# Optimization experiments

Measured on AMD Instinct MI355X. Metric: run time of the kernel, lower is better.

Reference implementation:

```python
import jax, jax.numpy as jnp
import numpy as np

N, E, G = 50000, 800000, 64
IN, HID, H, OUT = 128, 64, 4, 10


def _gat_layer(x, src, dst, W, a_src, a_dst, b):
    # x: [N, Fin]; W: [H*C, Fin]; a_src/a_dst: [H, C]; b: [H*C]
    n = x.shape[0]
    C = a_src.shape[1]
    h = (x @ W.T).reshape(n, H, C)                      # [N, H, C]
    e_src = jnp.einsum('nhc,hc->nh', h, a_src)          # [N, H]
    e_dst = jnp.einsum('nhc,hc->nh', h, a_dst)          # [N, H]
    logits = jax.nn.leaky_relu(e_src[src] + e_dst[dst], 0.2)  # [E', H]
    # segment softmax over destination node
    m = jax.ops.segment_max(logits, dst, num_segments=n)
    ex = jnp.exp(logits - m[dst])
    denom = jax.ops.segment_sum(ex, dst, num_segments=n)
    alpha = ex / (denom[dst] + 1e-16)                   # [E', H]
    msg = h[src] * alpha[:, :, None]                    # [E', H, C]
    out = jax.ops.segment_sum(msg, dst, num_segments=n) # [N, H, C]
    return out.reshape(n, H * C) + b


def setup_inputs() -> dict:
    key = jax.random.key(0)
    ks = jax.random.split(key, 20)
    x = jax.random.normal(ks[0], (N, IN), dtype=jnp.float32)
    edge_index = jax.random.randint(ks[1], (2, E), 0, N, dtype=jnp.int64)
    batch = jnp.sort(jax.random.randint(ks[2], (N,), 0, G, dtype=jnp.int64))

    def glorot(k, shape):
        fan = shape[-1]
        return jax.random.normal(k, shape, dtype=jnp.float32) / jnp.sqrt(jnp.float32(fan))

    ins = [IN, HID * H, HID * H]
    params = {}
    for i, fin in enumerate(ins, start=1):
        params[f'W{i}'] = glorot(ks[3 * i], (H * HID, fin))
        params[f'a_src{i}'] = glorot(ks[3 * i + 1], (H, HID))
        params[f'a_dst{i}'] = glorot(ks[3 * i + 2], (H, HID))
        params[f'b{i}'] = jnp.zeros((H * HID,), dtype=jnp.float32)
    params['Wl'] = glorot(ks[13], (OUT, H * HID))
    params['bl'] = jnp.zeros((OUT,), dtype=jnp.float32)
    return dict(x=x, edge_index=edge_index, batch=batch, **params)


def reference(x, edge_index, batch,
              W1, a_src1, a_dst1, b1,
              W2, a_src2, a_dst2, b2,
              W3, a_src3, a_dst3, b3,
              Wl, bl):
    n = x.shape[0]
    loops = jnp.arange(n, dtype=edge_index.dtype)
    src = jnp.concatenate([edge_index[0], loops])  # add self-loops (PyG default)
    dst = jnp.concatenate([edge_index[1], loops])

    h = jax.nn.elu(_gat_layer(x, src, dst, W1, a_src1, a_dst1, b1))
    h = jax.nn.elu(_gat_layer(h, src, dst, W2, a_src2, a_dst2, b2))
    h = _gat_layer(h, src, dst, W3, a_src3, a_dst3, b3)

    # global mean pool over graphs
    sums = jax.ops.segment_sum(h, batch, num_segments=G)          # [G, H*HID]
    counts = jax.ops.segment_sum(jnp.ones((n,), h.dtype), batch, num_segments=G)
    pooled = sums / jnp.maximum(counts, 1.0)[:, None]
    return pooled @ Wl.T + bl                                      # [G, OUT]
```

## Files before the change

### kernel.cpp

```cpp
#include <hip/hip_runtime.h>
#include <hip/hip_bf16.h>
#include <math.h>

#define NNODES 50000
#define NEDGES 800000
#define NGRAPH 64
#define FIN 128
#define HC 256
#define NHEAD 4
#define NOUT 10
#define ETOT (NEDGES + NNODES)
#define NB196 ((NNODES + 255) / 256)
#define BCAP 5376
#define S1CHUNK 4096
#define NBS1 ((ETOT + S1CHUNK - 1) / S1CHUNK)


typedef unsigned short u16;
typedef unsigned char u8;
typedef __attribute__((ext_vector_type(8))) short short8;
typedef __attribute__((ext_vector_type(4))) float f32x4;
typedef __attribute__((ext_vector_type(2))) float f32x2;

__device__ inline u16 f2b(float f) {
    union { float f; unsigned u; } v; v.f = f;
    unsigned r = v.u + 0x7FFF + ((v.u >> 16) & 1);
    return (u16)(r >> 16);
}
__device__ inline float b2f(u16 u) {
    union { unsigned u; float f; } v; v.u = ((unsigned)u) << 16; return v.f;
}

__device__ inline void gload_lds16(const void* g, void* l) {
    __builtin_amdgcn_global_load_lds(
        (const __attribute__((address_space(1))) unsigned*)g,
        (__attribute__((address_space(3))) unsigned*)l, 16, 0, 0);
}


#define CS0 (NNODES * FIN)
#define CS1 (HC * FIN)
#define CS2 (HC * HC)
#define NBCONV (((CS0 + CS1 + 2 * CS2) / 4 + 255) / 256)

__global__ void prep_kernel(const float* __restrict__ x, const float* __restrict__ W1,
                            const float* __restrict__ W2, const float* __restrict__ W3,
                            u16* __restrict__ xb, u16* __restrict__ w1b,
                            u16* __restrict__ w2b, u16* __restrict__ w3b) {
    int b = blockIdx.x;
    long i = (long)(b * 256 + threadIdx.x) * 4;
    if (i < CS0) {
        float4 v = *(const float4*)(x + i);
        ushort4 o;
        o.x = f2b(v.x); o.y = f2b(v.y); o.z = f2b(v.z); o.w = f2b(v.w);
        *(ushort4*)(xb + i) = o;
    } else if (i < CS0 + CS1) {
        long off = i - CS0;
        float4 v = *(const float4*)(W1 + off);
        ushort4 o;
        o.x = f2b(v.x); o.y = f2b(v.y); o.z = f2b(v.z); o.w = f2b(v.w);
        *(ushort4*)(w1b + off) = o;
    } else if (i < CS0 + CS1 + 2 * CS2) {
        const float* src; u16* dst; long off;
        if (i < CS0 + CS1 + CS2) { src = W2; dst = w2b; off = i - CS0 - CS1; }
        else                     { src = W3; dst = w3b; off = i - CS0 - CS1 - CS2; }
        float4 v = *(const float4*)(src + off);
        int row = (int)(off >> 8), col = (int)(off & 255);
        float vv[4] = {v.x, v.y, v.z, v.w};
        #pragma unroll
        for (int k = 0; k < 4; ++k) {
            int c = col + k;
            int pp = (c & ~63) | ((c & 15) << 2) | ((c >> 4) & 3);
            dst[row * 256 + pp] = f2b(vv[k]);
        }
    }
}


__global__ __launch_bounds__(256) void scatter1_kernel(const int* __restrict__ ei,
                                                       int* __restrict__ bcur,
                                                       unsigned* __restrict__ tmp) {
    __shared__ int hist[NB196];
    __shared__ int basec[NB196];
    int tid = threadIdx.x;
    int e0 = blockIdx.x * S1CHUNK;
    for (int i = tid; i < NB196; i += 256) hist[i] = 0;
    __syncthreads();
    int bkt[16], rnk[16];
    unsigned pk[16];
    #pragma unroll
    for (int k = 0; k < 16; ++k) {
        int e = e0 + k * 256 + tid;
        bkt[k] = -1;
        if (e < ETOT) {
            int src, dstn;
            if (e < NEDGES) { src = ei[e]; dstn = ei[NEDGES + e]; }
            else            { src = dstn = e - NEDGES; }
            int b = dstn >> 8;
            bkt[k] = b;
            rnk[k] = atomicAdd(&hist[b], 1);
            pk[k] = (unsigned)src | ((unsigned)(dstn & 255) << 16);
        }
    }
    __syncthreads();
    for (int i = tid; i < NB196; i += 256) {
        int h = hist[i];
        basec[i] = h ? atomicAdd(&bcur[i], h) : 0;
    }
    __syncthreads();
    #pragma unroll
    for (int k = 0; k < 16; ++k) {
        if (bkt[k] >= 0) {
            int pos = basec[bkt[k]] + rnk[k];
            if (pos < BCAP)
                tmp[(size_t)bkt[k] * BCAP + pos] = pk[k];
        }
    }
}


__global__ __launch_bounds__(256) void scanb_kernel(const int* __restrict__ bcur,
                                                    int* __restrict__ bsum,
                                                    const int* __restrict__ batch,
                                                    int* __restrict__ goff) {
    int tid = threadIdx.x, lane = tid & 63, wid = tid >> 6;
    __shared__ int ws[4];
    int v = 0;
    if (tid < NB196) { v = bcur[tid]; if (v > BCAP) v = BCAP; }
    int x = v;
    #pragma unroll
    for (int o = 1; o < 64; o <<= 1) {
        int t = __shfl_up(x, o);
        if (lane >= o) x += t;
    }
    if (lane == 63) ws[wid] = x;
    __syncthreads();
    if (tid < 4) {
        int w = ws[tid];
        #pragma unroll
        for (int o = 1; o < 4; o <<= 1) {
            int t = __shfl_up(w, o, 4);
            if ((tid & 3) >= o) w += t;
        }
        ws[tid] = w;
    }
    __syncthreads();
    int wexcl = wid ? ws[wid - 1] : 0;
    if (tid <= NB196) bsum[tid] = x - v + wexcl;
    if (tid <= NGRAPH) {
        int g = tid, lo = 0, hi = NNODES;
        while (lo < hi) {
            int mid = (lo + hi) >> 1;
            if (batch[mid] < g) lo = mid + 1; else hi = mid;
        }
        goff[g] = lo;
    }
}


__global__ __launch_bounds__(256) void scatter2_kernel(const unsigned* __restrict__ tmp,
                                                       const int* __restrict__ bcur,
                                                       const int* __restrict__ bsum,
                                                       int* __restrict__ off,
                                                       int* __restrict__ ssrc) {
    __shared__ unsigned ebuf[BCAP];
    __shared__ int ldss[BCAP];
    __shared__ int cnt[256];
    __shared__ int loff[256];
    __shared__ int ws[4];
    int b = blockIdx.x;
    int tid = threadIdx.x;
    int n = bcur[b];
    if (n > BCAP) n = BCAP;
    cnt[tid] = 0;
    const unsigned* tb = tmp + (size_t)b * BCAP;
    for (int i = tid; i < n; i += 256) ebuf[i] = tb[i];
    __syncthreads();
    for (int i = tid; i < n; i += 256) atomicAdd(&cnt[ebuf[i] >> 16], 1);
    __syncthreads();
    int lane = tid & 63, wid = tid >> 6;
    int v = cnt[tid];
    int x = v;
    #pragma unroll
    for (int o = 1; o < 64; o <<= 1) {
        int t = __shfl_up(x, o);
        if (lane >= o) x += t;
    }
    if (lane == 63) ws[wid] = x;
    __syncthreads();
    if (tid < 4) {
        int w = ws[tid];
        #pragma unroll
        for (int o = 1; o < 4; o <<= 1) {
            int t = __shfl_up(w, o, 4);
            if ((tid & 3) >= o) w += t;
        }
        ws[tid] = w;
    }
    __syncthreads();
    int wexcl = wid ? ws[wid - 1] : 0;
    int excl = x - v + wexcl;
    loff[tid] = excl;
    off[b * 256 + tid] = excl;
    cnt[tid] = 0;
    __syncthreads();
    for (int i = tid; i < n; i += 256) {
        unsigned pk = ebuf[i];
        int ld = (int)(pk >> 16);
        int rank = atomicAdd(&cnt[ld], 1);
        ldss[loff[ld] + rank] = (int)(pk & 0xFFFFu);
    }
    __syncthreads();
    int s = bsum[b];
    for (int i = tid; i < n; i += 256) ssrc[s + i] = ldss[i];
}


#define TBM 128
#define TBN 128
#define TBK 32

__global__ __launch_bounds__(256) void gemm_mfma(const u16* __restrict__ A,
                                                 const u16* __restrict__ B,
                                                 u8* __restrict__ C, int K,
                                                 const float* __restrict__ asrc,
                                                 const float* __restrict__ adst,
                                                 float* __restrict__ es,
                                                 float* __restrict__ ed) {
    __shared__ u16 Als[TBM * TBK];
    __shared__ u16 Bls[TBN * TBK];
    int tid = threadIdx.x;
    int wave = tid >> 6, lane = tid & 63;
    int brow = blockIdx.x * TBM, bcol = blockIdx.y * TBN;
    int m_base = (wave >> 1) * 64, n_base = (wave & 1) * 64;
    int r0 = tid >> 2, kc = (tid & 3) * 8;
    int lquad = lane >> 4, l16 = lane & 15;

    f32x4 acc[4][4] = {};

    const u16* ga0 = A + (size_t)(brow + r0) * K + kc;
    const u16* ga1 = A + (size_t)(brow + 64 + r0) * K + kc;
    const u16* gb0 = B + (size_t)(bcol + r0) * K + kc;
    const u16* gb1 = B + (size_t)(bcol + 64 + r0) * K + kc;
    u16* la0 = &Als[r0 * TBK + kc];
    u16* la1 = &Als[(64 + r0) * TBK + kc];
    u16* lb0 = &Bls[r0 * TBK + kc];
    u16* lb1 = &Bls[(64 + r0) * TBK + kc];

    for (int k0 = 0; k0 < K; k0 += TBK) {
        __syncthreads();
        gload_lds16(ga0 + k0, la0);
        gload_lds16(ga1 + k0, la1);
        gload_lds16(gb0 + k0, lb0);
        gload_lds16(gb1 + k0, lb1);
        __syncthreads();
        short8 fa[4], fb[4];
        #pragma unroll
        for (int i = 0; i < 4; ++i) {
            fa[i] = *(const short8*)(&Als[(m_base + i * 16 + l16) * TBK + lquad * 8]);
            fb[i] = *(const short8*)(&Bls[(n_base + i * 16 + l16) * TBK + lquad * 8]);
        }
        #pragma unroll
        for (int i = 0; i < 4; ++i)
            #pragma unroll
            for (int j = 0; j < 4; ++j)
                acc[i][j] = __builtin_amdgcn_mfma_f32_16x16x32_bf16(fa[i], fb[j], acc[i][j], 0, 0, 0);
    }

    #pragma unroll
    for (int i = 0; i < 4; ++i) {
        int rbase = brow + m_base + i * 16 + lquad * 4;
        #pragma unroll
        for (int r = 0; r < 4; ++r) {
            int row = rbase + r;
            if (row < NNODES) {
                int u = 0;
                u = __builtin_amdgcn_cvt_pk_fp8_f32(acc[i][0][r], acc[i][1][r], u, false);
                u = __builtin_amdgcn_cvt_pk_fp8_f32(acc[i][2][r], acc[i][3][r], u, true);
                *(int*)(C + (size_t)row * HC + bcol + n_base + l16 * 4) = u;
            }
        }
    }

    int head = (bcol + n_base) >> 6;
    float asv[4], adv[4];
    #pragma unroll
    for (int j = 0; j < 4; ++j) {
        asv[j] = asrc[head * 64 + j * 16 + l16];
        adv[j] = adst[head * 64 + j * 16 + l16];
    }
    #pragma unroll
    for (int i = 0; i < 4; ++i) {
        #pragma unroll
        for (int r = 0; r < 4; ++r) {
            float ps = 0.f, pd = 0.f;
            #pragma unroll
            for (int j = 0; j < 4; ++j) {
                ps = fmaf(acc[i][j][r], asv[j], ps);
                pd = fmaf(acc[i][j][r], adv[j], pd);
            }
            #pragma unroll
            for (int o = 1; o < 16; o <<= 1) {
                ps += __shfl_xor(ps, o);
                pd += __shfl_xor(pd, o);
            }
            int row = brow + m_base + i * 16 + lquad * 4 + r;
            if (l16 == 0 && row < NNODES) {
                es[row * 4 + head] = ps;
                ed[row * 4 + head] = pd;
            }
        }
    }
}


__global__ __launch_bounds__(256) void aggregate_kernel(const u8* __restrict__ h,
                                                        const int* __restrict__ ssrc,
                                                        const int* __restrict__ off,
                                                        const int* __restrict__ bsum,
                                                        const float* __restrict__ es,
                                                        const float* __restrict__ ed,
                                                        const float* __restrict__ bias,
                                                        u16* __restrict__ out,
                                                        int apply_elu) {
    __shared__ int2 xch[4][4][2][17];
    const unsigned* h32 = (const unsigned*)h;
    int wid = threadIdx.x >> 6;
    int dst = blockIdx.x * 4 + wid;
    if (dst >= NNODES) return;
    int lane = threadIdx.x & 63;
    int head = lane >> 4;
    int j16 = lane & 15;
    int s = off[dst] + bsum[dst >> 8];
    int e = off[dst + 1] + bsum[(dst + 1) >> 8];
    float edh = ed[dst * 4 + head];

    float a0 = 0.f, a1 = 0.f, a2 = 0.f, a3 = 0.f, dpriv = 0.f;

    {
        int cnt0 = e - s; if (cnt0 > 16) cnt0 = 16;
        int idx0 = s + j16; if (idx0 >= ETOT) idx0 = 0;
        int src0 = ssrc[idx0];
        float l = es[src0 * 4 + head] + edh;
        l = fmaxf(l, 0.2f * l);
        float ex0 = 0.f;
        if (j16 < cnt0) { ex0 = __expf(l); dpriv += ex0; }
        xch[wid][head][0][j16] = make_int2(src0, __float_as_int(ex0));
    }
    int nidx = s + 16 + j16; if (nidx >= ETOT) nidx = 0;
    int nsrc = ssrc[nidx];

    int buf = 0;
    for (int base = s; base < e; base += 16) {
        int cur = e - base; if (cur > 16) cur = 16;
        int nbase = base + 16;
        float esv = es[(unsigned)nsrc * 4 + head];
        int n2idx = base + 32 + j16; if (n2idx >= ETOT) n2idx = 0;
        int n2src = ssrc[n2idx];
        const int2* slot = &xch[wid][head][buf][0];
        for (int j = 0; j < cur; ++j) {
            int2 pr = slot[j];
            float exj = __int_as_float(pr.y);
            unsigned hv = h32[(unsigned)pr.x * 64 + lane];
            f32x2 lo = __builtin_amdgcn_cvt_pk_f32_fp8(hv, false);
            f32x2 hi = __builtin_amdgcn_cvt_pk_f32_fp8(hv, true);
            a0 += lo.x * exj;
            a1 += lo.y * exj;
            a2 += hi.x * exj;
            a3 += hi.y * exj;
        }
        if (nbase < e) {
            int ncnt = e - nbase; if (ncnt > 16) ncnt = 16;
            float l = esv + edh;
            l = fmaxf(l, 0.2f * l);
            float nex = 0.f;
            if (j16 < ncnt) { nex = __expf(l); dpriv += nex; }
            xch[wid][head][buf ^ 1][j16] = make_int2(nsrc, __float_as_int(nex));
        }
        nsrc = n2src;
        buf ^= 1;
    }

    #pragma unroll
    for (int o = 1; o < 16; o <<= 1) dpriv += __shfl_xor(dpriv, o);
    float inv = 1.f / (dpriv + 1e-16f);
    int bbase = ((lane >> 4) << 6) | (lane & 15);
    float b0 = bias[bbase], b1 = bias[bbase + 16], b2 = bias[bbase + 32], b3 = bias[bbase + 48];
    float o0 = a0 * inv + b0;
    float o1 = a1 * inv + b1;
    float o2 = a2 * inv + b2;
    float o3 = a3 * inv + b3;
    if (apply_elu) {
        o0 = o0 > 0.f ? o0 : __expf(o0) - 1.f;
        o1 = o1 > 0.f ? o1 : __expf(o1) - 1.f;
        o2 = o2 > 0.f ? o2 : __expf(o2) - 1.f;
        o3 = o3 > 0.f ? o3 : __expf(o3) - 1.f;
    }
    ushort4 ov;
    ov.x = f2b(o0); ov.y = f2b(o1); ov.z = f2b(o2); ov.w = f2b(o3);
    *(ushort4*)(out + (size_t)dst * HC + lane * 4) = ov;
}


__global__ __launch_bounds__(256) void pool_kernel(const u16* __restrict__ hin,
                                                   const int* __restrict__ goff,
                                                   float* __restrict__ pp) {
    int g = blockIdx.x;
    int slice = blockIdx.y;
    int lane = threadIdx.x & 63;
    int wid = threadIdx.x >> 6;
    int s = goff[g], e = goff[g + 1];
    float a0 = 0.f, a1 = 0.f, a2 = 0.f, a3 = 0.f;
    for (int n = s + slice * 4 + wid; n < e; n += 32) {
        ushort4 hv = *(const ushort4*)(hin + (size_t)n * HC + lane * 4);
        a0 += b2f(hv.x); a1 += b2f(hv.y); a2 += b2f(hv.z); a3 += b2f(hv.w);
    }
    __shared__ float4 part[4][64];
    part[wid][lane] = make_float4(a0, a1, a2, a3);
    __syncthreads();
    if (wid == 0) {
        float4 p0 = part[0][lane], p1 = part[1][lane], p2 = part[2][lane], p3 = part[3][lane];
        float4 v = make_float4((p0.x + p1.x) + (p2.x + p3.x),
                               (p0.y + p1.y) + (p2.y + p3.y),
                               (p0.z + p1.z) + (p2.z + p3.z),
                               (p0.w + p1.w) + (p2.w + p3.w));
        *(float4*)(pp + ((size_t)(g * 8 + slice)) * HC + lane * 4) = v;
    }
}


__global__ __launch_bounds__(64) void final_kernel(const float* __restrict__ pp,
                                                   const int* __restrict__ goff,
                                                   const float* __restrict__ Wl,
                                                   const float* __restrict__ bl,
                                                   float* __restrict__ out) {
    int g = blockIdx.x;
    int lane = threadIdx.x;
    float4 pv = make_float4(0.f, 0.f, 0.f, 0.f);
    #pragma unroll
    for (int sl = 0; sl < 8; ++sl) {
        float4 v = *(const float4*)(pp + ((size_t)(g * 8 + sl)) * HC + lane * 4);
        pv.x += v.x; pv.y += v.y; pv.z += v.z; pv.w += v.w;
    }
    float cntf = fmaxf((float)(goff[g + 1] - goff[g]), 1.f);
    float inv = 1.f / cntf;
    pv.x *= inv; pv.y *= inv; pv.z *= inv; pv.w *= inv;
    int wbase = ((lane >> 4) << 6) | (lane & 15);
    float acc[NOUT];
    #pragma unroll
    for (int o = 0; o < NOUT; ++o) {
        const float* w = Wl + o * HC + wbase;
        acc[o] = pv.x * w[0] + pv.y * w[16] + pv.z * w[32] + pv.w * w[48];
    }
    #pragma unroll
    for (int s = 32; s > 0; s >>= 1)
        #pragma unroll
        for (int o = 0; o < NOUT; ++o)
            acc[o] += __shfl_xor(acc[o], s);
    if (lane == 0) {
        #pragma unroll
        for (int o = 0; o < NOUT; ++o)
            out[g * NOUT + o] = acc[o] + bl[o];
    }
}


extern "C" void kernel_launch(void* const* d_in, const int* in_sizes, int n_in,
                              void* d_out, int out_size, void* d_ws, size_t ws_size,
                              hipStream_t stream) {
    (void)in_sizes; (void)n_in; (void)out_size; (void)ws_size;
    const float* x   = (const float*)d_in[0];
    const int*   ei  = (const int*)d_in[1];
    const int*   bat = (const int*)d_in[2];
    const float* W1  = (const float*)d_in[3];
    const float* as1 = (const float*)d_in[4];
    const float* ad1 = (const float*)d_in[5];
    const float* b1  = (const float*)d_in[6];
    const float* W2  = (const float*)d_in[7];
    const float* as2 = (const float*)d_in[8];
    const float* ad2 = (const float*)d_in[9];
    const float* b2  = (const float*)d_in[10];
    const float* W3  = (const float*)d_in[11];
    const float* as3 = (const float*)d_in[12];
    const float* ad3 = (const float*)d_in[13];
    const float* b3  = (const float*)d_in[14];
    const float* Wl  = (const float*)d_in[15];
    const float* bl  = (const float*)d_in[16];
    float* out = (float*)d_out;

    char* ws = (char*)d_ws;
    size_t p = 0;
    auto alloc = [&](size_t bytes) {
        size_t a = p;
        p += (bytes + 255) & ~(size_t)255;
        return a;
    };
    int*      off  = (int*)(ws + alloc((size_t)(NB196 * 256 + 256) * 4));
    int*      bcur = (int*)(ws + alloc(256 * 4));
    int*      ssrc = (int*)(ws + alloc((size_t)ETOT * 4));
    unsigned* tmp  = (unsigned*)(ws + alloc((size_t)NB196 * BCAP * 4));
    int*      bsum = (int*)(ws + alloc(256 * 4));
    float*    es   = (float*)(ws + alloc((size_t)NNODES * NHEAD * 4));
    float*    ed   = (float*)(ws + alloc((size_t)NNODES * NHEAD * 4));
    u16*      xb   = (u16*)(ws + alloc((size_t)NNODES * FIN * 2));
    u16*      w1b  = (u16*)(ws + alloc((size_t)HC * FIN * 2));
    u16*      w2b  = (u16*)(ws + alloc((size_t)HC * HC * 2));
    u16*      w3b  = (u16*)(ws + alloc((size_t)HC * HC * 2));
    u8*       Hb   = (u8*)(ws + alloc((size_t)NNODES * HC));
    u16*      Ab   = (u16*)(ws + alloc((size_t)NNODES * HC * 2));
    float*    pp   = (float*)(ws + alloc((size_t)NGRAPH * 8 * HC * 4));
    int*      goff = (int*)(ws + alloc((size_t)(NGRAPH + 1) * 4));
    alloc(128 * 1024);

    hipMemsetAsync(bcur, 0, 256 * 4, stream);

    prep_kernel<<<NBCONV, 256, 0, stream>>>(x, W1, W2, W3, xb, w1b, w2b, w3b);

    scatter1_kernel<<<NBS1, 256, 0, stream>>>(ei, bcur, tmp);
    scanb_kernel<<<1, 256, 0, stream>>>(bcur, bsum, bat, goff);
    scatter2_kernel<<<NB196, 256, 0, stream>>>(tmp, bcur, bsum, off, ssrc);

    dim3 ggrid((NNODES + TBM - 1) / TBM, HC / TBN);
    int nblocks4 = (NNODES + 3) / 4;

    gemm_mfma<<<ggrid, 256, 0, stream>>>(xb, w1b, Hb, FIN, as1, ad1, es, ed);
    aggregate_kernel<<<nblocks4, 256, 0, stream>>>(Hb, ssrc, off, bsum, es, ed, b1, Ab, 1);
    gemm_mfma<<<ggrid, 256, 0, stream>>>(Ab, w2b, Hb, HC, as2, ad2, es, ed);
    aggregate_kernel<<<nblocks4, 256, 0, stream>>>(Hb, ssrc, off, bsum, es, ed, b2, Ab, 1);
    gemm_mfma<<<ggrid, 256, 0, stream>>>(Ab, w3b, Hb, HC, as3, ad3, es, ed);
    aggregate_kernel<<<nblocks4, 256, 0, stream>>>(Hb, ssrc, off, bsum, es, ed, b3, Ab, 0);

    dim3 pgrid(NGRAPH, 8);
    pool_kernel<<<pgrid, 256, 0, stream>>>(Ab, goff, pp);
    final_kernel<<<NGRAPH, 64, 0, stream>>>(pp, goff, Wl, bl, out);
}
```

Before: 338.7 us.

## Split each destination's edge list across two wavefronts with LDS reduction

The aggregate kernel now assigns two wavefronts per destination node, each handling alternating 16-edge chunks, and combines partial accumulators and softmax denominators through shared memory after a block barrier. It also fully unrolls the inner gather loop for full chunks and uses packed two-wide float math for the accumulation. The aim is to shorten the serial dependent gather chain per node and raise memory-level parallelism, at the cost of a __syncthreads, extra LDS traffic, and half the wavefronts sitting idle in the epilogue. The grid is doubled to match.

Result: slower. 436.3 us (+28.8%).

```diff
diff --git a/kernel.cpp b/kernel.cpp
--- a/kernel.cpp
+++ b/kernel.cpp
@@ -324,10 +324,12 @@
                                                         u16* __restrict__ out,
                                                         int apply_elu) {
     __shared__ int2 xch[4][4][2][17];
+    __shared__ f32x4 part[4][64];
+    __shared__ float dsum[4][4];
     const unsigned* h32 = (const unsigned*)h;
     int wid = threadIdx.x >> 6;
-    int dst = blockIdx.x * 4 + wid;
-    if (dst >= NNODES) return;
+    int half = wid & 1;
+    int dst = blockIdx.x * 2 + (wid >> 1);
     int lane = threadIdx.x & 63;
     int head = lane >> 4;
     int j16 = lane & 15;
@@ -335,40 +337,55 @@
     int e = off[dst + 1] + bsum[(dst + 1) >> 8];
     float edh = ed[dst * 4 + head];
 
-    float a0 = 0.f, a1 = 0.f, a2 = 0.f, a3 = 0.f, dpriv = 0.f;
-
+    f32x2 a01 = {0.f, 0.f}, a23 = {0.f, 0.f};
+    float dpriv = 0.f;
+
+    int b0 = s + half * 16;
     {
-        int cnt0 = e - s; if (cnt0 > 16) cnt0 = 16;
-        int idx0 = s + j16; if (idx0 >= ETOT) idx0 = 0;
+        int cnt0 = e - b0; if (cnt0 > 16) cnt0 = 16;
+        int idx0 = b0 + j16; if (idx0 >= ETOT) idx0 = 0;
         int src0 = ssrc[idx0];
-        float l = es[src0 * 4 + head] + edh;
+        float l = es[(unsigned)src0 * 4 + head] + edh;
         l = fmaxf(l, 0.2f * l);
         float ex0 = 0.f;
         if (j16 < cnt0) { ex0 = __expf(l); dpriv += ex0; }
         xch[wid][head][0][j16] = make_int2(src0, __float_as_int(ex0));
     }
-    int nidx = s + 16 + j16; if (nidx >= ETOT) nidx = 0;
+    int nidx = b0 + 32 + j16; if (nidx >= ETOT) nidx = 0;
     int nsrc = ssrc[nidx];
 
     int buf = 0;
-    for (int base = s; base < e; base += 16) {
+    for (int base = b0; base < e; base += 32) {
         int cur = e - base; if (cur > 16) cur = 16;
-        int nbase = base + 16;
         float esv = es[(unsigned)nsrc * 4 + head];
-        int n2idx = base + 32 + j16; if (n2idx >= ETOT) n2idx = 0;
+        int n2idx = base + 64 + j16; if (n2idx >= ETOT) n2idx = 0;
         int n2src = ssrc[n2idx];
         const int2* slot = &xch[wid][head][buf][0];
-        for (int j = 0; j < cur; ++j) {
-            int2 pr = slot[j];
-            float exj = __int_as_float(pr.y);
-            unsigned hv = h32[(unsigned)pr.x * 64 + lane];
-            f32x2 lo = __builtin_amdgcn_cvt_pk_f32_fp8(hv, false);
-            f32x2 hi = __builtin_amdgcn_cvt_pk_f32_fp8(hv, true);
-            a0 += lo.x * exj;
-            a1 += lo.y * exj;
-            a2 += hi.x * exj;
-            a3 += hi.y * exj;
-        }
+        if (cur == 16) {
+            #pragma unroll
+            for (int j = 0; j < 16; ++j) {
+                int2 pr = slot[j];
+                float exj = __int_as_float(pr.y);
+                unsigned hv = h32[(unsigned)pr.x * 64 + lane];
+                f32x2 lo = __builtin_amdgcn_cvt_pk_f32_fp8(hv, false);
+                f32x2 hi = __builtin_amdgcn_cvt_pk_f32_fp8(hv, true);
+                f32x2 e2 = {exj, exj};
+                a01 += lo * e2;
+                a23 += hi * e2;
+            }
+        } else {
+            for (int j = 0; j < cur; ++j) {
+                int2 pr = slot[j];
+                float exj = __int_as_float(pr.y);
+                unsigned hv = h32[(unsigned)pr.x * 64 + lane];
+                f32x2 lo = __builtin_amdgcn_cvt_pk_f32_fp8(hv, false);
+                f32x2 hi = __builtin_amdgcn_cvt_pk_f32_fp8(hv, true);
+                f32x2 e2 = {exj, exj};
+                a01 += lo * e2;
+                a23 += hi * e2;
+            }
+        }
+        int nbase = base + 32;
         if (nbase < e) {
             int ncnt = e - nbase; if (ncnt > 16) ncnt = 16;
             float l = esv + edh;
@@ -383,22 +400,29 @@
 
     #pragma unroll
     for (int o = 1; o < 16; o <<= 1) dpriv += __shfl_xor(dpriv, o);
-    float inv = 1.f / (dpriv + 1e-16f);
-    int bbase = ((lane >> 4) << 6) | (lane & 15);
-    float b0 = bias[bbase], b1 = bias[bbase + 16], b2 = bias[bbase + 32], b3 = bias[bbase + 48];
-    float o0 = a0 * inv + b0;
-    float o1 = a1 * inv + b1;
-    float o2 = a2 * inv + b2;
-    float o3 = a3 * inv + b3;
-    if (apply_elu) {
-        o0 = o0 > 0.f ? o0 : __expf(o0) - 1.f;
-        o1 = o1 > 0.f ? o1 : __expf(o1) - 1.f;
-        o2 = o2 > 0.f ? o2 : __expf(o2) - 1.f;
-        o3 = o3 > 0.f ? o3 : __expf(o3) - 1.f;
-    }
-    ushort4 ov;
-    ov.x = f2b(o0); ov.y = f2b(o1); ov.z = f2b(o2); ov.w = f2b(o3);
-    *(ushort4*)(out + (size_t)dst * HC + lane * 4) = ov;
+    if (j16 == 0) dsum[wid][head] = dpriv;
+    f32x4 pv; pv[0] = a01.x; pv[1] = a01.y; pv[2] = a23.x; pv[3] = a23.y;
+    part[wid][lane] = pv;
+    __syncthreads();
+    if (half == 0) {
+        f32x4 p0 = part[wid][lane], p1 = part[wid + 1][lane];
+        float d = dsum[wid][head] + dsum[wid + 1][head];
+        float inv = 1.f / (d + 1e-16f);
+        int bbase = ((lane >> 4) << 6) | (lane & 15);
+        float o0 = (p0[0] + p1[0]) * inv + bias[bbase];
+        float o1 = (p0[1] + p1[1]) * inv + bias[bbase + 16];
+        float o2 = (p0[2] + p1[2]) * inv + bias[bbase + 32];
+        float o3 = (p0[3] + p1[3]) * inv + bias[bbase + 48];
+        if (apply_elu) {
+            o0 = o0 > 0.f ? o0 : __expf(o0) - 1.f;
+            o1 = o1 > 0.f ? o1 : __expf(o1) - 1.f;
+            o2 = o2 > 0.f ? o2 : __expf(o2) - 1.f;
+            o3 = o3 > 0.f ? o3 : __expf(o3) - 1.f;
+        }
+        ushort4 ov;
+        ov.x = f2b(o0); ov.y = f2b(o1); ov.z = f2b(o2); ov.w = f2b(o3);
+        *(ushort4*)(out + (size_t)dst * HC + lane * 4) = ov;
+    }
 }
 
 
@@ -521,14 +545,14 @@
     scatter2_kernel<<<NB196, 256, 0, stream>>>(tmp, bcur, bsum, off, ssrc);
 
     dim3 ggrid((NNODES + TBM - 1) / TBM, HC / TBN);
-    int nblocks4 = (NNODES + 3) / 4;
+    int nblocks2 = (NNODES + 1) / 2;
 
     gemm_mfma<<<ggrid, 256, 0, stream>>>(xb, w1b, Hb, FIN, as1, ad1, es, ed);
-    aggregate_kernel<<<nblocks4, 256, 0, stream>>>(Hb, ssrc, off, bsum, es, ed, b1, Ab, 1);
+    aggregate_kernel<<<nblocks2, 256, 0, stream>>>(Hb, ssrc, off, bsum, es, ed, b1, Ab, 1);
     gemm_mfma<<<ggrid, 256, 0, stream>>>(Ab, w2b, Hb, HC, as2, ad2, es, ed);
-    aggregate_kernel<<<nblocks4, 256, 0, stream>>>(Hb, ssrc, off, bsum, es, ed, b2, Ab, 1);
+    aggregate_kernel<<<nblocks2, 256, 0, stream>>>(Hb, ssrc, off, bsum, es, ed, b2, Ab, 1);
     gemm_mfma<<<ggrid, 256, 0, stream>>>(Ab, w3b, Hb, HC, as3, ad3, es, ed);
-    aggregate_kernel<<<nblocks4, 256, 0, stream>>>(Hb, ssrc, off, bsum, es, ed, b3, Ab, 0);
+    aggregate_kernel<<<nblocks2, 256, 0, stream>>>(Hb, ssrc, off, bsum, es, ed, b3, Ab, 0);
 
     dim3 pgrid(NGRAPH, 8);
     pool_kernel<<<pgrid, 256, 0, stream>>>(Ab, goff, pp);
```

## Process two destination nodes per wavefront in GAT aggregation with interleaved gathers

Applied to the files above, without the earlier changes.

Each wavefront in the aggregation kernel now handles two consecutive destination nodes, interleaving their edge-chunk loops so two independent gather streams are in flight at once. Full 16-edge chunks use an unrolled inner loop, and accumulation uses packed float2 multiply-adds. The goal is more memory-level parallelism and fewer loop overheads on the latency-bound feature gathers. In exchange it uses more registers and LDS per wave, and the grid is halved, which leaves less room for load balancing when the two nodes have very different degrees.

Result: slower. 353.4 us (+4.3%).

```diff
diff --git a/kernel.cpp b/kernel.cpp
--- a/kernel.cpp
+++ b/kernel.cpp
@@ -323,82 +323,161 @@
                                                         const float* __restrict__ bias,
                                                         u16* __restrict__ out,
                                                         int apply_elu) {
-    __shared__ int2 xch[4][4][2][17];
+    __shared__ int2 xch[4][2][4][2][17];
     const unsigned* h32 = (const unsigned*)h;
     int wid = threadIdx.x >> 6;
-    int dst = blockIdx.x * 4 + wid;
-    if (dst >= NNODES) return;
     int lane = threadIdx.x & 63;
     int head = lane >> 4;
     int j16 = lane & 15;
-    int s = off[dst] + bsum[dst >> 8];
-    int e = off[dst + 1] + bsum[(dst + 1) >> 8];
-    float edh = ed[dst * 4 + head];
-
-    float a0 = 0.f, a1 = 0.f, a2 = 0.f, a3 = 0.f, dpriv = 0.f;
+    int dstA = blockIdx.x * 8 + wid * 2;
+    int dstB = dstA + 1;
+    int sA = off[dstA] + bsum[dstA >> 8];
+    int eA = off[dstA + 1] + bsum[(dstA + 1) >> 8];
+    int sB = eA;
+    int eB = off[dstB + 1] + bsum[(dstB + 1) >> 8];
+    float edhA = ed[dstA * 4 + head];
+    float edhB = ed[dstB * 4 + head];
+
+    f32x2 a01A = {0.f, 0.f}, a23A = {0.f, 0.f};
+    f32x2 a01B = {0.f, 0.f}, a23B = {0.f, 0.f};
+    float dprA = 0.f, dprB = 0.f;
 
     {
-        int cnt0 = e - s; if (cnt0 > 16) cnt0 = 16;
-        int idx0 = s + j16; if (idx0 >= ETOT) idx0 = 0;
-        int src0 = ssrc[idx0];
-        float l = es[src0 * 4 + head] + edh;
-        l = fmaxf(l, 0.2f * l);
-        float ex0 = 0.f;
-        if (j16 < cnt0) { ex0 = __expf(l); dpriv += ex0; }
-        xch[wid][head][0][j16] = make_int2(src0, __float_as_int(ex0));
-    }
-    int nidx = s + 16 + j16; if (nidx >= ETOT) nidx = 0;
-    int nsrc = ssrc[nidx];
-
-    int buf = 0;
-    for (int base = s; base < e; base += 16) {
-        int cur = e - base; if (cur > 16) cur = 16;
-        int nbase = base + 16;
-        float esv = es[(unsigned)nsrc * 4 + head];
-        int n2idx = base + 32 + j16; if (n2idx >= ETOT) n2idx = 0;
-        int n2src = ssrc[n2idx];
-        const int2* slot = &xch[wid][head][buf][0];
-        for (int j = 0; j < cur; ++j) {
-            int2 pr = slot[j];
-            float exj = __int_as_float(pr.y);
-            unsigned hv = h32[(unsigned)pr.x * 64 + lane];
-            f32x2 lo = __builtin_amdgcn_cvt_pk_f32_fp8(hv, false);
-            f32x2 hi = __builtin_amdgcn_cvt_pk_f32_fp8(hv, true);
-            a0 += lo.x * exj;
-            a1 += lo.y * exj;
-            a2 += hi.x * exj;
-            a3 += hi.y * exj;
-        }
-        if (nbase < e) {
-            int ncnt = e - nbase; if (ncnt > 16) ncnt = 16;
-            float l = esv + edh;
-            l = fmaxf(l, 0.2f * l);
+        int i0A = sA + j16; if (i0A >= ETOT) i0A = 0;
+        int i0B = sB + j16; if (i0B >= ETOT) i0B = 0;
+        int srcA0 = ssrc[i0A];
+        int srcB0 = ssrc[i0B];
+        float lA = es[(unsigned)srcA0 * 4 + head] + edhA;
+        float lB = es[(unsigned)srcB0 * 4 + head] + edhB;
+        lA = fmaxf(lA, 0.2f * lA);
+        lB = fmaxf(lB, 0.2f * lB);
+        int cA0 = eA - sA; if (cA0 > 16) cA0 = 16;
+        int cB0 = eB - sB; if (cB0 > 16) cB0 = 16;
+        float exA = 0.f, exB = 0.f;
+        if (j16 < cA0) { exA = __expf(lA); dprA += exA; }
+        if (j16 < cB0) { exB = __expf(lB); dprB += exB; }
+        xch[wid][0][head][0][j16] = make_int2(srcA0, __float_as_int(exA));
+        xch[wid][1][head][0][j16] = make_int2(srcB0, __float_as_int(exB));
+    }
+    int niA = sA + 16 + j16; if (niA >= ETOT) niA = 0;
+    int niB = sB + 16 + j16; if (niB >= ETOT) niB = 0;
+    int nsrcA = ssrc[niA];
+    int nsrcB = ssrc[niB];
+
+    int baseA = sA, baseB = sB;
+    int bufA = 0, bufB = 0;
+    while (baseA < eA || baseB < eB) {
+        float esvA = es[(unsigned)nsrcA * 4 + head];
+        float esvB = es[(unsigned)nsrcB * 4 + head];
+        int n2A = baseA + 32 + j16; if (n2A >= ETOT) n2A = 0;
+        int n2B = baseB + 32 + j16; if (n2B >= ETOT) n2B = 0;
+        int n2srcA = ssrc[n2A];
+        int n2srcB = ssrc[n2B];
+        int curA = eA - baseA; if (curA > 16) curA = 16; if (curA < 0) curA = 0;
+        int curB = eB - baseB; if (curB > 16) curB = 16; if (curB < 0) curB = 0;
+        const int2* slA = &xch[wid][0][head][bufA][0];
+        const int2* slB = &xch[wid][1][head][bufB][0];
+        if (curA == 16) {
+            #pragma unroll
+            for (int j = 0; j < 16; ++j) {
+                int2 pr = slA[j];
+                float exj = __int_as_float(pr.y);
+                unsigned hv = h32[(unsigned)pr.x * 64 + lane];
+                f32x2 lo = __builtin_amdgcn_cvt_pk_f32_fp8(hv, false);
+                f32x2 hi = __builtin_amdgcn_cvt_pk_f32_fp8(hv, true);
+                f32x2 e2 = {exj, exj};
+                a01A += lo * e2;
+                a23A += hi * e2;
+            }
+        } else {
+            for (int j = 0; j < curA; ++j) {
+                int2 pr = slA[j];
+                float exj = __int_as_float(pr.y);
+                unsigned hv = h32[(unsigned)pr.x * 64 + lane];
+                f32x2 lo = __builtin_amdgcn_cvt_pk_f32_fp8(hv, false);
+                f32x2 hi = __builtin_amdgcn_cvt_pk_f32_fp8(hv, true);
+                f32x2 e2 = {exj, exj};
+                a01A += lo * e2;
+                a23A += hi * e2;
+            }
+        }
+        if (curB == 16) {
+            #pragma unroll
+            for (int j = 0; j < 16; ++j) {
+                int2 pr = slB[j];
+                float exj = __int_as_float(pr.y);
+                unsigned hv = h32[(unsigned)pr.x * 64 + lane];
+                f32x2 lo = __builtin_amdgcn_cvt_pk_f32_fp8(hv, false);
+                f32x2 hi = __builtin_amdgcn_cvt_pk_f32_fp8(hv, true);
+                f32x2 e2 = {exj, exj};
+                a01B += lo * e2;
+                a23B += hi * e2;
+            }
+        } else {
+            for (int j = 0; j < curB; ++j) {
+                int2 pr = slB[j];
+                float exj = __int_as_float(pr.y);
+                unsigned hv = h32[(unsigned)pr.x * 64 + lane];
+                f32x2 lo = __builtin_amdgcn_cvt_pk_f32_fp8(hv, false);
+                f32x2 hi = __builtin_amdgcn_cvt_pk_f32_fp8(hv, true);
+                f32x2 e2 = {exj, exj};
+                a01B += lo * e2;
+                a23B += hi * e2;
+            }
+        }
+        int nbA = baseA + 16, nbB = baseB + 16;
+        if (nbA < eA) {
+            int nc = eA - nbA; if (nc > 16) nc = 16;
+            float l = esvA + edhA; l = fmaxf(l, 0.2f * l);
             float nex = 0.f;
-            if (j16 < ncnt) { nex = __expf(l); dpriv += nex; }
-            xch[wid][head][buf ^ 1][j16] = make_int2(nsrc, __float_as_int(nex));
-        }
-        nsrc = n2src;
-        buf ^= 1;
-    }
-
-    #pragma unroll
-    for (int o = 1; o < 16; o <<= 1) dpriv += __shfl_xor(dpriv, o);
-    float inv = 1.f / (dpriv + 1e-16f);
+            if (j16 < nc) { nex = __expf(l); dprA += nex; }
+            xch[wid][0][head][bufA ^ 1][j16] = make_int2(nsrcA, __float_as_int(nex));
+        }
+        if (nbB < eB) {
+            int nc = eB - nbB; if (nc > 16) nc = 16;
+            float l = esvB + edhB; l = fmaxf(l, 0.2f * l);
+            float nex = 0.f;
+            if (j16 < nc) { nex = __expf(l); dprB += nex; }
+            xch[wid][1][head][bufB ^ 1][j16] = make_int2(nsrcB, __float_as_int(nex));
+        }
+        nsrcA = n2srcA; nsrcB = n2srcB;
+        bufA ^= 1; bufB ^= 1;
+        baseA = nbA; baseB = nbB;
+    }
+
+    #pragma unroll
+    for (int o = 1; o < 16; o <<= 1) {
+        dprA += __shfl_xor(dprA, o);
+        dprB += __shfl_xor(dprB, o);
+    }
+    float invA = 1.f / (dprA + 1e-16f);
+    float invB = 1.f / (dprB + 1e-16f);
     int bbase = ((lane >> 4) << 6) | (lane & 15);
     float b0 = bias[bbase], b1 = bias[bbase + 16], b2 = bias[bbase + 32], b3 = bias[bbase + 48];
-    float o0 = a0 * inv + b0;
-    float o1 = a1 * inv + b1;
-    float o2 = a2 * inv + b2;
-    float o3 = a3 * inv + b3;
+
+    float o0 = a01A.x * invA + b0;
+    float o1 = a01A.y * invA + b1;
+    float o2 = a23A.x * invA + b2;
+    float o3 = a23A.y * invA + b3;
+    float p0 = a01B.x * invB + b0;
+    float p1 = a01B.y * invB + b1;
+    float p2 = a23B.x * invB + b2;
+    float p3 = a23B.y * invB + b3;
     if (apply_elu) {
         o0 = o0 > 0.f ? o0 : __expf(o0) - 1.f;
         o1 = o1 > 0.f ? o1 : __expf(o1) - 1.f;
         o2 = o2 > 0.f ? o2 : __expf(o2) - 1.f;
         o3 = o3 > 0.f ? o3 : __expf(o3) - 1.f;
-    }
-    ushort4 ov;
-    ov.x = f2b(o0); ov.y = f2b(o1); ov.z = f2b(o2); ov.w = f2b(o3);
-    *(ushort4*)(out + (size_t)dst * HC + lane * 4) = ov;
+        p0 = p0 > 0.f ? p0 : __expf(p0) - 1.f;
+        p1 = p1 > 0.f ? p1 : __expf(p1) - 1.f;
+        p2 = p2 > 0.f ? p2 : __expf(p2) - 1.f;
+        p3 = p3 > 0.f ? p3 : __expf(p3) - 1.f;
+    }
+    ushort4 ovA, ovB;
+    ovA.x = f2b(o0); ovA.y = f2b(o1); ovA.z = f2b(o2); ovA.w = f2b(o3);
+    ovB.x = f2b(p0); ovB.y = f2b(p1); ovB.z = f2b(p2); ovB.w = f2b(p3);
+    *(ushort4*)(out + (size_t)dstA * HC + lane * 4) = ovA;
+    *(ushort4*)(out + (size_t)dstB * HC + lane * 4) = ovB;
 }
 
 
@@ -521,14 +600,14 @@
     scatter2_kernel<<<NB196, 256, 0, stream>>>(tmp, bcur, bsum, off, ssrc);
 
     dim3 ggrid((NNODES + TBM - 1) / TBM, HC / TBN);
-    int nblocks4 = (NNODES + 3) / 4;
+    int nblocks8 = NNODES / 8;
 
     gemm_mfma<<<ggrid, 256, 0, stream>>>(xb, w1b, Hb, FIN, as1, ad1, es, ed);
-    aggregate_kernel<<<nblocks4, 256, 0, stream>>>(Hb, ssrc, off, bsum, es, ed, b1, Ab, 1);
+    aggregate_kernel<<<nblocks8, 256, 0, stream>>>(Hb, ssrc, off, bsum, es, ed, b1, Ab, 1);
     gemm_mfma<<<ggrid, 256, 0, stream>>>(Ab, w2b, Hb, HC, as2, ad2, es, ed);
-    aggregate_kernel<<<nblocks4, 256, 0, stream>>>(Hb, ssrc, off, bsum, es, ed, b2, Ab, 1);
+    aggregate_kernel<<<nblocks8, 256, 0, stream>>>(Hb, ssrc, off, bsum, es, ed, b2, Ab, 1);
     gemm_mfma<<<ggrid, 256, 0, stream>>>(Ab, w3b, Hb, HC, as3, ad3, es, ed);
-    aggregate_kernel<<<nblocks4, 256, 0, stream>>>(Hb, ssrc, off, bsum, es, ed, b3, Ab, 0);
+    aggregate_kernel<<<nblocks8, 256, 0, stream>>>(Hb, ssrc, off, bsum, es, ed, b3, Ab, 0);
 
     dim3 pgrid(NGRAPH, 8);
     pool_kernel<<<pgrid, 256, 0, stream>>>(Ab, goff, pp);
```

## Merge prep and scatter launches, fold bucket scan into scatter2, simplify aggregate loop

Applied to the files above, without the earlier changes.

Fuses the bf16 conversion kernel and the first scatter pass into one launch. The single-block scan kernel is removed: each scatter2 block recomputes the global bucket prefix and writes absolute offsets, and pool/final compute graph bounds by binary search on batch. The aggregate kernel's double-buffered software prefetch of source indices is replaced by a simpler full-chunk loop plus a tail, which drops the extra bsum lookup but gives up load prefetching. The aim is to cut launch and serialization overhead from small kernels.

Result: no change. 342.9 us (+1.2%).

```diff
diff --git a/kernel.cpp b/kernel.cpp
--- a/kernel.cpp
+++ b/kernel.cpp
@@ -37,53 +37,64 @@
         (__attribute__((address_space(3))) unsigned*)l, 16, 0, 0);
 }
 
+__device__ inline int lbound(const int* __restrict__ batch, int g) {
+    int lo = 0, hi = NNODES;
+    while (lo < hi) {
+        int mid = (lo + hi) >> 1;
+        if (batch[mid] < g) lo = mid + 1; else hi = mid;
+    }
+    return lo;
+}
+
 
 #define CS0 (NNODES * FIN)
 #define CS1 (HC * FIN)
 #define CS2 (HC * HC)
 #define NBCONV (((CS0 + CS1 + 2 * CS2) / 4 + 255) / 256)
 
-__global__ void prep_kernel(const float* __restrict__ x, const float* __restrict__ W1,
-                            const float* __restrict__ W2, const float* __restrict__ W3,
-                            u16* __restrict__ xb, u16* __restrict__ w1b,
-                            u16* __restrict__ w2b, u16* __restrict__ w3b) {
-    int b = blockIdx.x;
-    long i = (long)(b * 256 + threadIdx.x) * 4;
-    if (i < CS0) {
-        float4 v = *(const float4*)(x + i);
-        ushort4 o;
-        o.x = f2b(v.x); o.y = f2b(v.y); o.z = f2b(v.z); o.w = f2b(v.w);
-        *(ushort4*)(xb + i) = o;
-    } else if (i < CS0 + CS1) {
-        long off = i - CS0;
-        float4 v = *(const float4*)(W1 + off);
-        ushort4 o;
-        o.x = f2b(v.x); o.y = f2b(v.y); o.z = f2b(v.z); o.w = f2b(v.w);
-        *(ushort4*)(w1b + off) = o;
-    } else if (i < CS0 + CS1 + 2 * CS2) {
-        const float* src; u16* dst; long off;
-        if (i < CS0 + CS1 + CS2) { src = W2; dst = w2b; off = i - CS0 - CS1; }
-        else                     { src = W3; dst = w3b; off = i - CS0 - CS1 - CS2; }
-        float4 v = *(const float4*)(src + off);
-        int row = (int)(off >> 8), col = (int)(off & 255);
-        float vv[4] = {v.x, v.y, v.z, v.w};
-        #pragma unroll
-        for (int k = 0; k < 4; ++k) {
-            int c = col + k;
-            int pp = (c & ~63) | ((c & 15) << 2) | ((c >> 4) & 3);
-            dst[row * 256 + pp] = f2b(vv[k]);
-        }
-    }
-}
-
-
-__global__ __launch_bounds__(256) void scatter1_kernel(const int* __restrict__ ei,
-                                                       int* __restrict__ bcur,
-                                                       unsigned* __restrict__ tmp) {
+__global__ __launch_bounds__(256) void prep_kernel(const float* __restrict__ x,
+                                                   const float* __restrict__ W1,
+                                                   const float* __restrict__ W2,
+                                                   const float* __restrict__ W3,
+                                                   u16* __restrict__ xb, u16* __restrict__ w1b,
+                                                   u16* __restrict__ w2b, u16* __restrict__ w3b,
+                                                   const int* __restrict__ ei,
+                                                   int* __restrict__ bcur,
+                                                   unsigned* __restrict__ tmp) {
     __shared__ int hist[NB196];
     __shared__ int basec[NB196];
+    int b = blockIdx.x;
+    if (b < NBCONV) {
+        long i = (long)(b * 256 + threadIdx.x) * 4;
+        if (i < CS0) {
+            float4 v = *(const float4*)(x + i);
+            ushort4 o;
+            o.x = f2b(v.x); o.y = f2b(v.y); o.z = f2b(v.z); o.w = f2b(v.w);
+            *(ushort4*)(xb + i) = o;
+        } else if (i < CS0 + CS1) {
+            long off = i - CS0;
+            float4 v = *(const float4*)(W1 + off);
+            ushort4 o;
+            o.x = f2b(v.x); o.y = f2b(v.y); o.z = f2b(v.z); o.w = f2b(v.w);
+            *(ushort4*)(w1b + off) = o;
+        } else if (i < CS0 + CS1 + 2 * CS2) {
+            const float* src; u16* dst; long off;
+            if (i < CS0 + CS1 + CS2) { src = W2; dst = w2b; off = i - CS0 - CS1; }
+            else                     { src = W3; dst = w3b; off = i - CS0 - CS1 - CS2; }
+            float4 v = *(const float4*)(src + off);
+            int row = (int)(off >> 8), col = (int)(off & 255);
+            float vv[4] = {v.x, v.y, v.z, v.w};
+            #pragma unroll
+            for (int k = 0; k < 4; ++k) {
+                int c = col + k;
+                int pp = (c & ~63) | ((c & 15) << 2) | ((c >> 4) & 3);
+                dst[row * 256 + pp] = f2b(vv[k]);
+            }
+        }
+        return;
+    }
     int tid = threadIdx.x;
-    int e0 = blockIdx.x * S1CHUNK;
+    int e0 = (b - NBCONV) * S1CHUNK;
     for (int i = tid; i < NB196; i += 256) hist[i] = 0;
     __syncthreads();
     int bkt[16], rnk[16];
@@ -96,9 +107,9 @@
             int src, dstn;
             if (e < NEDGES) { src = ei[e]; dstn = ei[NEDGES + e]; }
             else            { src = dstn = e - NEDGES; }
-            int b = dstn >> 8;
-            bkt[k] = b;
-            rnk[k] = atomicAdd(&hist[b], 1);
+            int bb = dstn >> 8;
+            bkt[k] = bb;
+            rnk[k] = atomicAdd(&hist[bb], 1);
             pk[k] = (unsigned)src | ((unsigned)(dstn & 255) << 16);
         }
     }
@@ -119,48 +130,8 @@
 }
 
 
-__global__ __launch_bounds__(256) void scanb_kernel(const int* __restrict__ bcur,
-                                                    int* __restrict__ bsum,
-                                                    const int* __restrict__ batch,
-                                                    int* __restrict__ goff) {
-    int tid = threadIdx.x, lane = tid & 63, wid = tid >> 6;
-    __shared__ int ws[4];
-    int v = 0;
-    if (tid < NB196) { v = bcur[tid]; if (v > BCAP) v = BCAP; }
-    int x = v;
-    #pragma unroll
-    for (int o = 1; o < 64; o <<= 1) {
-        int t = __shfl_up(x, o);
-        if (lane >= o) x += t;
-    }
-    if (lane == 63) ws[wid] = x;
-    __syncthreads();
-    if (tid < 4) {
-        int w = ws[tid];
-        #pragma unroll
-        for (int o = 1; o < 4; o <<= 1) {
-            int t = __shfl_up(w, o, 4);
-            if ((tid & 3) >= o) w += t;
-        }
-        ws[tid] = w;
-    }
-    __syncthreads();
-    int wexcl = wid ? ws[wid - 1] : 0;
-    if (tid <= NB196) bsum[tid] = x - v + wexcl;
-    if (tid <= NGRAPH) {
-        int g = tid, lo = 0, hi = NNODES;
-        while (lo < hi) {
-            int mid = (lo + hi) >> 1;
-            if (batch[mid] < g) lo = mid + 1; else hi = mid;
-        }
-        goff[g] = lo;
-    }
-}
-
-
 __global__ __launch_bounds__(256) void scatter2_kernel(const unsigned* __restrict__ tmp,
                                                        const int* __restrict__ bcur,
-                                                       const int* __restrict__ bsum,
                                                        int* __restrict__ off,
                                                        int* __restrict__ ssrc) {
     __shared__ unsigned ebuf[BCAP];
@@ -168,17 +139,47 @@
     __shared__ int cnt[256];
     __shared__ int loff[256];
     __shared__ int ws[4];
+    __shared__ int sbase;
     int b = blockIdx.x;
     int tid = threadIdx.x;
+    int lane = tid & 63, wid = tid >> 6;
+
+    int bv = 0;
+    if (tid < NB196) { bv = bcur[tid]; if (bv > BCAP) bv = BCAP; }
+    {
+        int x = bv;
+        #pragma unroll
+        for (int o = 1; o < 64; o <<= 1) {
+            int t = __shfl_up(x, o);
+            if (lane >= o) x += t;
+        }
+        if (lane == 63) ws[wid] = x;
+        __syncthreads();
+        if (tid < 4) {
+            int w = ws[tid];
+            #pragma unroll
+            for (int o = 1; o < 4; o <<= 1) {
+                int t = __shfl_up(w, o, 4);
+                if ((tid & 3) >= o) w += t;
+            }
+            ws[tid] = w;
+        }
+        __syncthreads();
+        int wexcl = wid ? ws[wid - 1] : 0;
+        int gexcl = x - bv + wexcl;
+        if (tid == b) sbase = gexcl;
+        __syncthreads();
+    }
+    int s = sbase;
     int n = bcur[b];
     if (n > BCAP) n = BCAP;
+
     cnt[tid] = 0;
     const unsigned* tb = tmp + (size_t)b * BCAP;
     for (int i = tid; i < n; i += 256) ebuf[i] = tb[i];
     __syncthreads();
     for (int i = tid; i < n; i += 256) atomicAdd(&cnt[ebuf[i] >> 16], 1);
     __syncthreads();
-    int lane = tid & 63, wid = tid >> 6;
     int v = cnt[tid];
     int x = v;
     #pragma unroll
@@ -201,7 +202,7 @@
     int wexcl = wid ? ws[wid - 1] : 0;
     int excl = x - v + wexcl;
     loff[tid] = excl;
-    off[b * 256 + tid] = excl;
+    off[b * 256 + tid] = s + excl;
     cnt[tid] = 0;
     __syncthreads();
     for (int i = tid; i < n; i += 256) {
@@ -211,7 +212,6 @@
         ldss[loff[ld] + rank] = (int)(pk & 0xFFFFu);
     }
     __syncthreads();
-    int s = bsum[b];
     for (int i = tid; i < n; i += 256) ssrc[s + i] = ldss[i];
 }
 
@@ -317,13 +317,12 @@
 __global__ __launch_bounds__(256) void aggregate_kernel(const u8* __restrict__ h,
                                                         const int* __restrict__ ssrc,
                                                         const int* __restrict__ off,
-                                                        const int* __restrict__ bsum,
                                                         const float* __restrict__ es,
                                                         const float* __restrict__ ed,
                                                         const float* __restrict__ bias,
                                                         u16* __restrict__ out,
                                                         int apply_elu) {
-    __shared__ int2 xch[4][4][2][17];
+    __shared__ int2 xch[4][4][17];
     const unsigned* h32 = (const unsigned*)h;
     int wid = threadIdx.x >> 6;
     int dst = blockIdx.x * 4 + wid;
@@ -331,35 +330,24 @@
     int lane = threadIdx.x & 63;
     int head = lane >> 4;
     int j16 = lane & 15;
-    int s = off[dst] + bsum[dst >> 8];
-    int e = off[dst + 1] + bsum[(dst + 1) >> 8];
+    int s = off[dst];
+    int e = off[dst + 1];
     float edh = ed[dst * 4 + head];
+    int2* myslot = &xch[wid][head][0];
 
     float a0 = 0.f, a1 = 0.f, a2 = 0.f, a3 = 0.f, dpriv = 0.f;
 
-    {
-        int cnt0 = e - s; if (cnt0 > 16) cnt0 = 16;
-        int idx0 = s + j16; if (idx0 >= ETOT) idx0 = 0;
-        int src0 = ssrc[idx0];
-        float l = es[src0 * 4 + head] + edh;
+    int base = s;
+    for (; base + 16 <= e; base += 16) {
+        int mysrc = ssrc[base + j16];
+        float l = es[mysrc * 4 + head] + edh;
         l = fmaxf(l, 0.2f * l);
-        float ex0 = 0.f;
-        if (j16 < cnt0) { ex0 = __expf(l); dpriv += ex0; }
-        xch[wid][head][0][j16] = make_int2(src0, __float_as_int(ex0));
-    }
-    int nidx = s + 16 + j16; if (nidx >= ETOT) nidx = 0;
-    int nsrc = ssrc[nidx];
-
-    int buf = 0;
-    for (int base = s; base < e; base += 16) {
-        int cur = e - base; if (cur > 16) cur = 16;
-        int nbase = base + 16;
-        float esv = es[(unsigned)nsrc * 4 + head];
-        int n2idx = base + 32 + j16; if (n2idx >= ETOT) n2idx = 0;
-        int n2src = ssrc[n2idx];
-        const int2* slot = &xch[wid][head][buf][0];
-        for (int j = 0; j < cur; ++j) {
-            int2 pr = slot[j];
+        float myex = __expf(l);
+        dpriv += myex;
+        myslot[j16] = make_int2(mysrc, __float_as_int(myex));
+        #pragma unroll
+        for (int j = 0; j < 16; ++j) {
+            int2 pr = myslot[j];
             float exj = __int_as_float(pr.y);
             unsigned hv = h32[(unsigned)pr.x * 64 + lane];
             f32x2 lo = __builtin_amdgcn_cvt_pk_f32_fp8(hv, false);
@@ -369,18 +357,30 @@
             a2 += hi.x * exj;
             a3 += hi.y * exj;
         }
-        if (nbase < e) {
-            int ncnt = e - nbase; if (ncnt > 16) ncnt = 16;
-            float l = esv + edh;
+    }
+    int cnt = e - base;
+    if (cnt > 0) {
+        int mysrc = 0; float myex = 0.f;
+        if (j16 < cnt) {
+            mysrc = ssrc[base + j16];
+            float l = es[mysrc * 4 + head] + edh;
             l = fmaxf(l, 0.2f * l);
-            float nex = 0.f;
-            if (j16 < ncnt) { nex = __expf(l); dpriv += nex; }
-            xch[wid][head][buf ^ 1][j16] = make_int2(nsrc, __float_as_int(nex));
-        }
-        nsrc = n2src;
-        buf ^= 1;
-    }
-
+            myex = __expf(l);
+            dpriv += myex;
+        }
+        myslot[j16] = make_int2(mysrc, __float_as_int(myex));
+        for (int j = 0; j < cnt; ++j) {
+            int2 pr = myslot[j];
+            float exj = __int_as_float(pr.y);
+            unsigned hv = h32[(unsigned)pr.x * 64 + lane];
+            f32x2 lo = __builtin_amdgcn_cvt_pk_f32_fp8(hv, false);
+            f32x2 hi = __builtin_amdgcn_cvt_pk_f32_fp8(hv, true);
+            a0 += lo.x * exj;
+            a1 += lo.y * exj;
+            a2 += hi.x * exj;
+            a3 += hi.y * exj;
+        }
+    }
     #pragma unroll
     for (int o = 1; o < 16; o <<= 1) dpriv += __shfl_xor(dpriv, o);
     float inv = 1.f / (dpriv + 1e-16f);
@@ -403,13 +403,13 @@
 
 
 __global__ __launch_bounds__(256) void pool_kernel(const u16* __restrict__ hin,
-                                                   const int* __restrict__ goff,
+                                                   const int* __restrict__ batch,
                                                    float* __restrict__ pp) {
     int g = blockIdx.x;
     int slice = blockIdx.y;
     int lane = threadIdx.x & 63;
     int wid = threadIdx.x >> 6;
-    int s = goff[g], e = goff[g + 1];
+    int s = lbound(batch, g), e = lbound(batch, g + 1);
     float a0 = 0.f, a1 = 0.f, a2 = 0.f, a3 = 0.f;
     for (int n = s + slice * 4 + wid; n < e; n += 32) {
         ushort4 hv = *(const ushort4*)(hin + (size_t)n * HC + lane * 4);
@@ -430,7 +430,7 @@
 
 
 __global__ __launch_bounds__(64) void final_kernel(const float* __restrict__ pp,
-                                                   const int* __restrict__ goff,
+                                                   const int* __restrict__ batch,
                                                    const float* __restrict__ Wl,
                                                    const float* __restrict__ bl,
                                                    float* __restrict__ out) {
@@ -442,7 +442,8 @@
         float4 v = *(const float4*)(pp + ((size_t)(g * 8 + sl)) * HC + lane * 4);
         pv.x += v.x; pv.y += v.y; pv.z += v.z; pv.w += v.w;
     }
-    float cntf = fmaxf((float)(goff[g + 1] - goff[g]), 1.f);
+    int cs = lbound(batch, g), ce = lbound(batch, g + 1);
+    float cntf = fmaxf((float)(ce - cs), 1.f);
     float inv = 1.f / cntf;
     pv.x *= inv; pv.y *= inv; pv.z *= inv; pv.w *= inv;
     int wbase = ((lane >> 4) << 6) | (lane & 15);
@@ -499,7 +500,6 @@
     int*      bcur = (int*)(ws + alloc(256 * 4));
     int*      ssrc = (int*)(ws + alloc((size_t)ETOT * 4));
     unsigned* tmp  = (unsigned*)(ws + alloc((size_t)NB196 * BCAP * 4));
-    int*      bsum = (int*)(ws + alloc(256 * 4));
     float*    es   = (float*)(ws + alloc((size_t)NNODES * NHEAD * 4));
     float*    ed   = (float*)(ws + alloc((size_t)NNODES * NHEAD * 4));
     u16*      xb   = (u16*)(ws + alloc((size_t)NNODES * FIN * 2));
@@ -509,28 +509,25 @@
     u8*       Hb   = (u8*)(ws + alloc((size_t)NNODES * HC));
     u16*      Ab   = (u16*)(ws + alloc((size_t)NNODES * HC * 2));
     float*    pp   = (float*)(ws + alloc((size_t)NGRAPH * 8 * HC * 4));
-    int*      goff = (int*)(ws + alloc((size_t)(NGRAPH + 1) * 4));
     alloc(128 * 1024);
 
     hipMemsetAsync(bcur, 0, 256 * 4, stream);
 
-    prep_kernel<<<NBCONV, 256, 0, stream>>>(x, W1, W2, W3, xb, w1b, w2b, w3b);
-
-    scatter1_kernel<<<NBS1, 256, 0, stream>>>(ei, bcur, tmp);
-    scanb_kernel<<<1, 256, 0, stream>>>(bcur, bsum, bat, goff);
-    scatter2_kernel<<<NB196, 256, 0, stream>>>(tmp, bcur, bsum, off, ssrc);
+    prep_kernel<<<NBCONV + NBS1, 256, 0, stream>>>(x, W1, W2, W3, xb, w1b, w2b, w3b,
+                                                   ei, bcur, tmp);
+    scatter2_kernel<<<NB196, 256, 0, stream>>>(tmp, bcur, off, ssrc);
 
     dim3 ggrid((NNODES + TBM - 1) / TBM, HC / TBN);
     int nblocks4 = (NNODES + 3) / 4;
 
     gemm_mfma<<<ggrid, 256, 0, stream>>>(xb, w1b, Hb, FIN, as1, ad1, es, ed);
-    aggregate_kernel<<<nblocks4, 256, 0, stream>>>(Hb, ssrc, off, bsum, es, ed, b1, Ab, 1);
+    aggregate_kernel<<<nblocks4, 256, 0, stream>>>(Hb, ssrc, off, es, ed, b1, Ab, 1);
     gemm_mfma<<<ggrid, 256, 0, stream>>>(Ab, w2b, Hb, HC, as2, ad2, es, ed);
-    aggregate_kernel<<<nblocks4, 256, 0, stream>>>(Hb, ssrc, off, bsum, es, ed, b2, Ab, 1);
+    aggregate_kernel<<<nblocks4, 256, 0, stream>>>(Hb, ssrc, off, es, ed, b2, Ab, 1);
     gemm_mfma<<<ggrid, 256, 0, stream>>>(Ab, w3b, Hb, HC, as3, ad3, es, ed);
-    aggregate_kernel<<<nblocks4, 256, 0, stream>>>(Hb, ssrc, off, bsum, es, ed, b3, Ab, 0);
+    aggregate_kernel<<<nblocks4, 256, 0, stream>>>(Hb, ssrc, off, es, ed, b3, Ab, 0);
 
     dim3 pgrid(NGRAPH, 8);
-    pool_kernel<<<pgrid, 256, 0, stream>>>(Ab, goff, pp);
-    final_kernel<<<NGRAPH, 64, 0, stream>>>(pp, goff, Wl, bl, out);
-}
+    pool_kernel<<<pgrid, 256, 0, stream>>>(Ab, bat, pp);
+    final_kernel<<<NGRAPH, 64, 0, stream>>>(pp, bat, Wl, bl, out);
+}
```
